# Kernel tuning notes

Measured on AMD Instinct MI355X. Metric: run time of the kernel, lower is better.

The kernel has to match this reference:

```python
import jax, jax.numpy as jnp
import numpy as np

S = 64.0  # scale
M = 0.35  # margin


def setup_inputs() -> dict:
    key = jax.random.key(0)
    k1, k2 = jax.random.split(key)
    B, C = 1024, 100000
    x = jax.random.uniform(k1, (B, C), dtype=jnp.float32)  # cosine-like logits in [0,1)
    label = jax.random.randint(k2, (B,), 0, C, dtype=jnp.int64)
    return {"x": x, "label": label}


def reference(x, label):
    B = x.shape[0]
    rows = jnp.arange(B)
    x_y = x[rows, label]                      # [B] target logit per sample
    numerator = S * (x_y - M)                 # margin-adjusted, scaled
    exp_sx = jnp.exp(S * x)                   # [B, C] single elementwise pass
    # sum over j != label  ==  full row sum minus the target term
    sum_excl = jnp.sum(exp_sx, axis=1) - jnp.exp(S * x_y)
    denominator = jnp.exp(numerator) + sum_excl
    L = (numerator - jnp.log(denominator)) / S
    return -jnp.mean(L)
```

## Files before the change

### kernel.cpp

```cpp
#include <hip/hip_runtime.h>
#include <math.h>


#define SCALE 64.0f
#define MARGIN 0.35f

__device__ __forceinline__ double block_reduce_d(double v) {
    #pragma unroll
    for (int off = 32; off > 0; off >>= 1) v += __shfl_down(v, off, 64);
    __shared__ double s[4];
    const int lane = threadIdx.x & 63;
    const int w    = threadIdx.x >> 6;
    if (lane == 0) s[w] = v;
    __syncthreads();
    if (w == 0) {
        v = (lane < 4) ? s[lane] : 0.0;
        v += __shfl_down(v, 2, 64);
        v += __shfl_down(v, 1, 64);
    }
    return v;
}

__global__ __launch_bounds__(256) void row_loss_kernel(
    const float* __restrict__ x, const int* __restrict__ label,
    double* __restrict__ row_L, int C)
{
    const int row = blockIdx.x;
    const float* __restrict__ xr = x + (size_t)row * (size_t)C;
    const int tid = threadIdx.x;

    const int n4 = C >> 2;
    const float4* __restrict__ x4 = (const float4*)xr;

    double acc = 0.0;
    int v = tid;
    for (; v + 3 * 256 < n4; v += 4 * 256) {
        float4 a = x4[v];
        float4 b = x4[v + 256];
        float4 c = x4[v + 512];
        float4 d = x4[v + 768];
        float s0 = __expf(SCALE * a.x) + __expf(SCALE * a.y) +
                   __expf(SCALE * a.z) + __expf(SCALE * a.w);
        float s1 = __expf(SCALE * b.x) + __expf(SCALE * b.y) +
                   __expf(SCALE * b.z) + __expf(SCALE * b.w);
        float s2 = __expf(SCALE * c.x) + __expf(SCALE * c.y) +
                   __expf(SCALE * c.z) + __expf(SCALE * c.w);
        float s3 = __expf(SCALE * d.x) + __expf(SCALE * d.y) +
                   __expf(SCALE * d.z) + __expf(SCALE * d.w);
        acc += (double)(s0 + s1) + (double)(s2 + s3);
    }
    for (; v < n4; v += 256) {
        float4 a = x4[v];
        float s0 = __expf(SCALE * a.x) + __expf(SCALE * a.y) +
                   __expf(SCALE * a.z) + __expf(SCALE * a.w);
        acc += (double)s0;
    }
    for (int j = (n4 << 2) + tid; j < C; j += 256)
        acc += (double)__expf(SCALE * xr[j]);

    double row_sum = block_reduce_d(acc);

    if (tid == 0) {
        const double xy  = (double)xr[label[row]];
        const double num = 64.0 * (xy - 0.35);
        const double exy = exp(64.0 * xy);
        const double sum_excl = row_sum - exy;
        const double denom = exp(num) + sum_excl;
        const double L = (num - log(denom)) / 64.0;
        row_L[row] = L;
    }
}

__global__ __launch_bounds__(256) void final_reduce_kernel(
    const double* __restrict__ row_L, float* __restrict__ out, int B)
{
    double acc = 0.0;
    for (int i = threadIdx.x; i < B; i += 256) acc += row_L[i];
    double total = block_reduce_d(acc);
    if (threadIdx.x == 0) out[0] = (float)(-total / (double)B);
}

extern "C" void kernel_launch(void* const* d_in, const int* in_sizes, int n_in,
                              void* d_out, int out_size, void* d_ws, size_t ws_size,
                              hipStream_t stream) {
    const float* x     = (const float*)d_in[0];
    const int*   label = (const int*)d_in[1];
    const int B = in_sizes[1];
    const int C = in_sizes[0] / B;

    double* row_L = (double*)d_ws;

    row_loss_kernel<<<B, 256, 0, stream>>>(x, label, row_L, C);
    final_reduce_kernel<<<1, 256, 0, stream>>>(row_L, (float*)d_out, B);
}
```

Measured before the change: 509.5 us.

## Split each row across multiple blocks and use native exp2 with float accumulation

Each row is now split into 8 chunks handled by separate blocks, which write double partial sums. A single finalize kernel combines the partials, computes the per-row loss and takes the mean. The inner loop now calls the hardware exp2 builtin with a prescaled constant and accumulates in float instead of double, which cuts per-element arithmetic. The aim is more parallelism for the memory-bound pass and less ALU work per element, at the cost of some precision in the float accumulation and a serial finalize over all rows.

```diff
diff --git a/kernel.cpp b/kernel.cpp
--- a/kernel.cpp
+++ b/kernel.cpp
@@ -2,8 +2,8 @@
 #include <math.h>
 
 
-#define SCALE 64.0f
-#define MARGIN 0.35f
+#define SPLIT 8
+#define EXP2(v) __builtin_amdgcn_exp2f(v)
 
 __device__ __forceinline__ double block_reduce_d(double v) {
     #pragma unroll
@@ -21,61 +21,69 @@
     return v;
 }
 
-__global__ __launch_bounds__(256) void row_loss_kernel(
+__global__ __launch_bounds__(256) void partial_sum_kernel(
+    const float* __restrict__ x, double* __restrict__ partials,
+    int C, int chunk)
+{
+    const int row  = blockIdx.x / SPLIT;
+    const int ch   = blockIdx.x - row * SPLIT;
+    const long off = (long)ch * chunk;
+    int n = C - (int)off;
+    if (n > chunk) n = chunk;
+    const int tid = threadIdx.x;
+    const float K2 = 92.33248261689366f;
+
+    float acc = 0.0f;
+    if (n > 0) {
+        const float* __restrict__ xp = x + (long)row * C + off;
+        const int n4 = n >> 2;
+        const float4* __restrict__ x4 = (const float4*)xp;
+
+        int v = tid;
+        for (; v + 3 * 256 < n4; v += 4 * 256) {
+            float4 a = x4[v];
+            float4 b = x4[v + 256];
+            float4 c = x4[v + 512];
+            float4 d = x4[v + 768];
+            float s0 = EXP2(K2 * a.x) + EXP2(K2 * a.y) +
+                       EXP2(K2 * a.z) + EXP2(K2 * a.w);
+            float s1 = EXP2(K2 * b.x) + EXP2(K2 * b.y) +
+                       EXP2(K2 * b.z) + EXP2(K2 * b.w);
+            float s2 = EXP2(K2 * c.x) + EXP2(K2 * c.y) +
+                       EXP2(K2 * c.z) + EXP2(K2 * c.w);
+            float s3 = EXP2(K2 * d.x) + EXP2(K2 * d.y) +
+                       EXP2(K2 * d.z) + EXP2(K2 * d.w);
+            acc += (s0 + s1) + (s2 + s3);
+        }
+        for (; v < n4; v += 256) {
+            float4 a = x4[v];
+            acc += EXP2(K2 * a.x) + EXP2(K2 * a.y) +
+                   EXP2(K2 * a.z) + EXP2(K2 * a.w);
+        }
+        for (int j = (n4 << 2) + tid; j < n; j += 256)
+            acc += EXP2(K2 * xp[j]);
+    }
+
+    double total = block_reduce_d((double)acc);
+    if (tid == 0) partials[(long)row * SPLIT + ch] = total;
+}
+
+__global__ __launch_bounds__(256) void finalize_kernel(
     const float* __restrict__ x, const int* __restrict__ label,
-    double* __restrict__ row_L, int C)
+    const double* __restrict__ partials, float* __restrict__ out,
+    int B, int C)
 {
-    const int row = blockIdx.x;
-    const float* __restrict__ xr = x + (size_t)row * (size_t)C;
-    const int tid = threadIdx.x;
-
-    const int n4 = C >> 2;
-    const float4* __restrict__ x4 = (const float4*)xr;
-
     double acc = 0.0;
-    int v = tid;
-    for (; v + 3 * 256 < n4; v += 4 * 256) {
-        float4 a = x4[v];
-        float4 b = x4[v + 256];
-        float4 c = x4[v + 512];
-        float4 d = x4[v + 768];
-        float s0 = __expf(SCALE * a.x) + __expf(SCALE * a.y) +
-                   __expf(SCALE * a.z) + __expf(SCALE * a.w);
-        float s1 = __expf(SCALE * b.x) + __expf(SCALE * b.y) +
-                   __expf(SCALE * b.z) + __expf(SCALE * b.w);
-        float s2 = __expf(SCALE * c.x) + __expf(SCALE * c.y) +
-                   __expf(SCALE * c.z) + __expf(SCALE * c.w);
-        float s3 = __expf(SCALE * d.x) + __expf(SCALE * d.y) +
-                   __expf(SCALE * d.z) + __expf(SCALE * d.w);
-        acc += (double)(s0 + s1) + (double)(s2 + s3);
-    }
-    for (; v < n4; v += 256) {
-        float4 a = x4[v];
-        float s0 = __expf(SCALE * a.x) + __expf(SCALE * a.y) +
-                   __expf(SCALE * a.z) + __expf(SCALE * a.w);
-        acc += (double)s0;
-    }
-    for (int j = (n4 << 2) + tid; j < C; j += 256)
-        acc += (double)__expf(SCALE * xr[j]);
-
-    double row_sum = block_reduce_d(acc);
-
-    if (tid == 0) {
-        const double xy  = (double)xr[label[row]];
+    for (int r = threadIdx.x; r < B; r += 256) {
+        double s = 0.0;
+        #pragma unroll
+        for (int c = 0; c < SPLIT; ++c) s += partials[(long)r * SPLIT + c];
+        const double xy  = (double)x[(long)r * C + label[r]];
         const double num = 64.0 * (xy - 0.35);
         const double exy = exp(64.0 * xy);
-        const double sum_excl = row_sum - exy;
-        const double denom = exp(num) + sum_excl;
-        const double L = (num - log(denom)) / 64.0;
-        row_L[row] = L;
+        const double denom = exp(num) + (s - exy);
+        acc += (num - log(denom)) * (1.0 / 64.0);
     }
-}
-
-__global__ __launch_bounds__(256) void final_reduce_kernel(
-    const double* __restrict__ row_L, float* __restrict__ out, int B)
-{
-    double acc = 0.0;
-    for (int i = threadIdx.x; i < B; i += 256) acc += row_L[i];
     double total = block_reduce_d(acc);
     if (threadIdx.x == 0) out[0] = (float)(-total / (double)B);
 }
@@ -88,8 +96,11 @@
     const int B = in_sizes[1];
     const int C = in_sizes[0] / B;
 
-    double* row_L = (double*)d_ws;
+    int chunk = (C + SPLIT - 1) / SPLIT;
+    chunk = (chunk + 3) & ~3;
 
-    row_loss_kernel<<<B, 256, 0, stream>>>(x, label, row_L, C);
-    final_reduce_kernel<<<1, 256, 0, stream>>>(row_L, (float*)d_out, B);
+    double* partials = (double*)d_ws;
+
+    partial_sum_kernel<<<B * SPLIT, 256, 0, stream>>>(x, partials, C, chunk);
+    finalize_kernel<<<1, 256, 0, stream>>>(x, label, partials, (float*)d_out, B, C);
 }
```

Result: slower. 531.4 us (+4.3%).
